# Performance work log

Measured on AMD Instinct MI355X. Metric: run time of the kernel, lower is better.

The kernel has to match this reference:

```python
import jax, jax.numpy as jnp
import numpy as np

MAX_DEPTH = 83.0
PI = 3.1415926535
SCALE = 8
FOCAL = 715.0

def setup_inputs() -> dict:
    key = jax.random.key(0)
    ks = jax.random.split(key, 16)
    B, C, H, W = 16, 128, 44, 152
    x = jax.random.normal(ks[0], (B, C, H, W), dtype=jnp.float32)
    # reduction 1x1 convs: 128->64->32->16->8->4
    chans = [128, 64, 32, 16, 8, 4]
    inp = {"x": x}
    for i in range(5):
        cin, cout = chans[i], chans[i + 1]
        w = jax.random.normal(ks[1 + 2 * i], (cout, cin), dtype=jnp.float32) * (1.0 / np.sqrt(cin))
        b = jax.random.normal(ks[2 + 2 * i], (cout,), dtype=jnp.float32) * 0.01
        inp[f"w{i}"] = w
        inp[f"b{i}"] = b
    # final 1x1 conv: 4 -> 3
    inp["cw"] = jax.random.normal(ks[11], (3, 4), dtype=jnp.float32) * 0.5
    inp["cb"] = jax.random.normal(ks[12], (3,), dtype=jnp.float32) * 0.01
    return inp

def _lpg_block(x, w0, b0, w1, b1, w2, b2, w3, b3, w4, b4, cw, cb):
    # reduction chain: 1x1 conv + ELU
    for w, b in ((w0, b0), (w1, b1), (w2, b2), (w3, b3), (w4, b4)):
        x = jax.nn.elu(jnp.einsum('oc,bchw->bohw', w, x) + b[None, :, None, None])
    # 4 -> 3 conv producing (theta, phi, dist) logits
    y = jnp.einsum('oc,bchw->bohw', cw, x) + cb[None, :, None, None]
    theta = jax.nn.sigmoid(y[:, 0]) * PI / 6.0          # [B,H,W]
    phi = jax.nn.sigmoid(y[:, 1]) * PI * 2.0
    dist = jax.nn.sigmoid(y[:, 2]) * MAX_DEPTH
    n1 = jnp.sin(theta) * jnp.cos(phi)
    n2 = jnp.sin(theta) * jnp.sin(phi)
    n3 = jnp.cos(theta)
    n = jnp.stack([n1, n2, n3], axis=1)                  # [B,3,H,W]
    # F.normalize(p=2, dim=1, eps=1e-12)
    norm = jnp.sqrt(jnp.sum(n * n, axis=1, keepdims=True))
    n = n / jnp.maximum(norm, 1e-12)
    n1, n2, n3 = n[:, 0], n[:, 1], n[:, 2]
    # LPG expansion: depth[b, y*s+ii, x*s+jj] = dist / (n1*u[jj] + n2*v[ii] + n3)
    s = SCALE
    off = (jnp.arange(s, dtype=jnp.float32) - (s - 1) / 2.0) / s / FOCAL  # [s]
    v = off[:, None]   # rows (ii)
    u = off[None, :]   # cols (jj)
    denom = (n1[..., None, None] * u + n2[..., None, None] * v
             + n3[..., None, None])                       # [B,H,W,s,s]
    depth = dist[..., None, None] / denom                 # [B,H,W,s,s]
    B, H, W = dist.shape
    depth = jnp.transpose(depth, (0, 1, 3, 2, 4)).reshape(B, 1, H * s, W * s)
    return depth

def reference(x, w0, b0, w1, b1, w2, b2, w3, b3, w4, b4, cw, cb):
    return _lpg_block(x, w0, b0, w1, b1, w2, b2, w3, b3, w4, b4, cw, cb)
```

## Files before the change

### kernel.cpp

```cpp
#include <hip/hip_runtime.h>
#include <math.h>

#define HW_   6688
#define W_    152
#define NPIX  107008
#define OW_   1216
#define OHW_  428032

typedef _Float16 f16;
typedef _Float16 f16x2 __attribute__((ext_vector_type(2)));
typedef _Float16 f16x4 __attribute__((ext_vector_type(4)));
typedef _Float16 f16x8 __attribute__((ext_vector_type(8)));
typedef float    f32x4 __attribute__((ext_vector_type(4)));

#define MFMA(a,b,c) __builtin_amdgcn_mfma_f32_16x16x32_f16((a),(b),(c),0,0,0)

#define SXH_STR  72
#define SA1_STR  40
#define SA2_OFF  5120
#define SA2_STR  24
#define SA3_OFF  8192
#define SA3_STR  16
#define SA0_OFF  10240
#define SA0_STR  72
#define LDSF16   19456

__device__ __forceinline__ float fast_sigmoid(float v) {
    return __builtin_amdgcn_rcpf(1.0f + __expf(-v));
}
__device__ __forceinline__ float eluf(float v) {
    return v > 0.0f ? v : (__expf(v) - 1.0f);
}
__device__ __forceinline__ void split8(const float* v, f16x8& hi, f16x8& lo) {
#pragma unroll
    for (int e = 0; e < 8; ++e) {
        f16 h = (f16)v[e];
        hi[e] = h;
        lo[e] = (f16)(v[e] - (float)h);
    }
}
__device__ __forceinline__ f16x4 elu_cvt4(f32x4 a) {
    f16x4 r;
    r[0] = (f16)eluf(a[0]); r[1] = (f16)eluf(a[1]);
    r[2] = (f16)eluf(a[2]); r[3] = (f16)eluf(a[3]);
    return r;
}
__device__ __forceinline__ void wave_fence() {
    __builtin_amdgcn_sched_barrier(0);
    __builtin_amdgcn_wave_barrier();
    __builtin_amdgcn_sched_barrier(0);
}
__device__ __forceinline__ void stage32(const float* __restrict__ xp, f16* dst) {
#pragma unroll 8
    for (int k = 0; k < 32; k += 2) {
        float v0 = xp[(size_t)k * HW_];
        float v1 = xp[(size_t)(k + 1) * HW_];
        f16x2 h; h[0] = (f16)v0; h[1] = (f16)v1;
        *(f16x2*)(dst + k) = h;
    }
}

__global__ __launch_bounds__(256, 4)
void lpg_mfma(const float* __restrict__ x,
              const float* __restrict__ w0, const float* __restrict__ b0,
              const float* __restrict__ w1, const float* __restrict__ b1,
              const float* __restrict__ w2, const float* __restrict__ b2,
              const float* __restrict__ w3, const float* __restrict__ b3,
              const float* __restrict__ w4, const float* __restrict__ b4,
              const float* __restrict__ cw, const float* __restrict__ cb,
              float* __restrict__ out) {
    __shared__ __align__(16) f16 S[LDSF16];
    f16* SX  = S;
    f16* SA0 = S + SA0_OFF;

    const int tid  = threadIdx.x;
    const int wv   = __builtin_amdgcn_readfirstlane(tid >> 6);
    const int lane = tid & 63;
    const int p    = lane & 15;
    const int q    = lane >> 4;
    const int pixbase = blockIdx.x * 128;

    const int i    = tid & 127;
    const int csub = (tid >> 7) * 32;
    int pixs = pixbase + i;
    int bbs  = pixs / HW_;
    int hws  = pixs - bbs * HW_;
    const float* xps = x + ((size_t)bbs * 128 + csub) * HW_ + hws;
    f16* dsts = SX + i * SXH_STR + csub;

    stage32(xps, dsts);

    const int w0row = (wv * 16 + p) * 128 + q * 8;
    f16x8 w0h[2], w0l[2];
#pragma unroll
    for (int kt = 0; kt < 2; ++kt) {
        float v[8];
#pragma unroll
        for (int e = 0; e < 8; ++e) v[e] = w0[w0row + kt * 32 + e];
        split8(v, w0h[kt], w0l[kt]);
    }
    f32x4 acc[8];
    {
        f32x4 b0v = *(const f32x4*)(b0 + wv * 16 + 4 * q);
#pragma unroll
        for (int t = 0; t < 8; ++t) acc[t] = b0v;
    }
    __syncthreads();

#pragma unroll 2
    for (int t = 0; t < 8; ++t) {
        const f16* bp = SX + (t * 16 + p) * SXH_STR + q * 8;
        f16x8 bf0 = *(const f16x8*)(bp);
        f16x8 bf1 = *(const f16x8*)(bp + 32);
        acc[t] = MFMA(w0h[0], bf0, acc[t]); acc[t] = MFMA(w0l[0], bf0, acc[t]);
        acc[t] = MFMA(w0h[1], bf1, acc[t]); acc[t] = MFMA(w0l[1], bf1, acc[t]);
    }
    __syncthreads();

    stage32(xps + (size_t)64 * HW_, dsts);
#pragma unroll
    for (int kt = 0; kt < 2; ++kt) {
        float v[8];
#pragma unroll
        for (int e = 0; e < 8; ++e) v[e] = w0[w0row + 64 + kt * 32 + e];
        split8(v, w0h[kt], w0l[kt]);
    }
    __syncthreads();

#pragma unroll 2
    for (int t = 0; t < 8; ++t) {
        const f16* bp = SX + (t * 16 + p) * SXH_STR + q * 8;
        f16x8 bf0 = *(const f16x8*)(bp);
        f16x8 bf1 = *(const f16x8*)(bp + 32);
        acc[t] = MFMA(w0h[0], bf0, acc[t]); acc[t] = MFMA(w0l[0], bf0, acc[t]);
        acc[t] = MFMA(w0h[1], bf1, acc[t]); acc[t] = MFMA(w0l[1], bf1, acc[t]);
        *(f16x4*)(SA0 + (t * 16 + p) * SA0_STR + wv * 16 + 4 * q) = elu_cvt4(acc[t]);
    }
    __syncthreads();

    f16x8 w1h[2][2], w1l[2][2];
#pragma unroll
    for (int Mt = 0; Mt < 2; ++Mt)
#pragma unroll
        for (int kt = 0; kt < 2; ++kt) {
            float v[8];
#pragma unroll
            for (int e = 0; e < 8; ++e) v[e] = w1[(Mt * 16 + p) * 64 + kt * 32 + q * 8 + e];
            split8(v, w1h[Mt][kt], w1l[Mt][kt]);
        }
    f16x8 w2h, w2l;
    {
        float v[8];
#pragma unroll
        for (int e = 0; e < 8; ++e) v[e] = w2[p * 32 + q * 8 + e];
        split8(v, w2h, w2l);
    }
    f16x8 w3h, w3l;
    {
        float v[8];
        bool ok = (p < 8) && (q < 2);
#pragma unroll
        for (int e = 0; e < 8; ++e) v[e] = ok ? w3[p * 16 + q * 8 + e] : 0.0f;
        split8(v, w3h, w3l);
    }
    f16x8 w4h, w4l;
    {
        float v[8];
        bool ok = (p < 4) && (q == 0);
#pragma unroll
        for (int e = 0; e < 8; ++e) v[e] = ok ? w4[p * 8 + e] : 0.0f;
        split8(v, w4h, w4l);
    }
    f16x8 whh, whl;
    {
        float v[8];
        bool ok = (p < 3) && (q == 0);
#pragma unroll
        for (int e = 0; e < 8; ++e) v[e] = (ok && e < 4) ? cw[p * 4 + e] : 0.0f;
        split8(v, whh, whl);
    }
    const f32x4 z4 = {0.f, 0.f, 0.f, 0.f};
    f32x4 b1v0 = *(const f32x4*)(b1 + 4 * q);
    f32x4 b1v1 = *(const f32x4*)(b1 + 16 + 4 * q);
    f32x4 b2v  = *(const f32x4*)(b2 + 4 * q);
    f32x4 b3v  = *(const f32x4*)(b3 + (q & 1) * 4);
    f32x4 b4v  = *(const f32x4*)(b4);
    float cb0v = cb[0], cb1v = cb[1], cb2v = cb[2];

    const int i0a = wv * 32 + p;
    const int i0b = wv * 32 + 16 + p;

    {
        f32x4 cA0 = b1v0, cA1 = b1v1, cB0 = b1v0, cB1 = b1v1;
#pragma unroll
        for (int kt = 0; kt < 2; ++kt) {
            f16x8 bfA = *(const f16x8*)(SA0 + i0a * SA0_STR + kt * 32 + q * 8);
            f16x8 bfB = *(const f16x8*)(SA0 + i0b * SA0_STR + kt * 32 + q * 8);
            cA0 = MFMA(w1h[0][kt], bfA, cA0); cA0 = MFMA(w1l[0][kt], bfA, cA0);
            cA1 = MFMA(w1h[1][kt], bfA, cA1); cA1 = MFMA(w1l[1][kt], bfA, cA1);
            cB0 = MFMA(w1h[0][kt], bfB, cB0); cB0 = MFMA(w1l[0][kt], bfB, cB0);
            cB1 = MFMA(w1h[1][kt], bfB, cB1); cB1 = MFMA(w1l[1][kt], bfB, cB1);
        }
        *(f16x4*)(SX + i0a * SA1_STR + 4 * q)      = elu_cvt4(cA0);
        *(f16x4*)(SX + i0a * SA1_STR + 16 + 4 * q) = elu_cvt4(cA1);
        *(f16x4*)(SX + i0b * SA1_STR + 4 * q)      = elu_cvt4(cB0);
        *(f16x4*)(SX + i0b * SA1_STR + 16 + 4 * q) = elu_cvt4(cB1);
    }
    wave_fence();

    {
        f16x8 bfA = *(const f16x8*)(SX + i0a * SA1_STR + q * 8);
        f16x8 bfB = *(const f16x8*)(SX + i0b * SA1_STR + q * 8);
        f32x4 cA = b2v, cB = b2v;
        cA = MFMA(w2h, bfA, cA); cA = MFMA(w2l, bfA, cA);
        cB = MFMA(w2h, bfB, cB); cB = MFMA(w2l, bfB, cB);
        *(f16x4*)(SX + SA2_OFF + i0a * SA2_STR + 4 * q) = elu_cvt4(cA);
        *(f16x4*)(SX + SA2_OFF + i0b * SA2_STR + 4 * q) = elu_cvt4(cB);
    }
    wave_fence();

    {
        f16x8 bfA = *(const f16x8*)(SX + SA2_OFF + i0a * SA2_STR + (q & 1) * 8);
        f16x8 bfB = *(const f16x8*)(SX + SA2_OFF + i0b * SA2_STR + (q & 1) * 8);
        if (q >= 2) { bfA = (f16x8){}; bfB = (f16x8){}; }
        f32x4 cA = (q < 2) ? b3v : z4, cB = (q < 2) ? b3v : z4;
        cA = MFMA(w3h, bfA, cA); cA = MFMA(w3l, bfA, cA);
        cB = MFMA(w3h, bfB, cB); cB = MFMA(w3l, bfB, cB);
        if (q < 2) {
            *(f16x4*)(SX + SA3_OFF + i0a * SA3_STR + 4 * q) = elu_cvt4(cA);
            *(f16x4*)(SX + SA3_OFF + i0b * SA3_STR + 4 * q) = elu_cvt4(cB);
        }
    }
    wave_fence();

    f32x4 cyA, cyB;
    {
        f16x8 bfA = *(const f16x8*)(SX + SA3_OFF + i0a * SA3_STR);
        f16x8 bfB = *(const f16x8*)(SX + SA3_OFF + i0b * SA3_STR);
        if (q != 0) { bfA = (f16x8){}; bfB = (f16x8){}; }
        f32x4 cA = (q == 0) ? b4v : z4, cB = (q == 0) ? b4v : z4;
        cA = MFMA(w4h, bfA, cA); cA = MFMA(w4l, bfA, cA);
        cB = MFMA(w4h, bfB, cB); cB = MFMA(w4l, bfB, cB);

        f16x8 hA = (f16x8){}, hB = (f16x8){};
        if (q == 0) {
#pragma unroll
            for (int e = 0; e < 4; ++e) {
                hA[e] = (f16)eluf(cA[e]);
                hB[e] = (f16)eluf(cB[e]);
            }
        }
        cyA = z4; cyB = z4;
        if (q == 0) {
            cyA[0] = cb0v; cyA[1] = cb1v; cyA[2] = cb2v;
            cyB[0] = cb0v; cyB[1] = cb1v; cyB[2] = cb2v;
        }
        cyA = MFMA(whh, hA, cyA); cyA = MFMA(whl, hA, cyA);
        cyB = MFMA(whh, hB, cyB); cyB = MFMA(whl, hB, cyB);
    }

#pragma unroll
    for (int nt = 0; nt < 2; ++nt) {
        const int i0 = wv * 32 + nt * 16 + p;
        float y0 = __shfl(nt ? cyB[0] : cyA[0], p);
        float y1 = __shfl(nt ? cyB[1] : cyA[1], p);
        float y2 = __shfl(nt ? cyB[2] : cyA[2], p);

        float theta = 0.5235987756f * fast_sigmoid(y0);
        float phi   = 6.2831853072f * fast_sigmoid(y1);
        float dist  = 83.0f         * fast_sigmoid(y2);
        float st = __sinf(theta), ct = __cosf(theta);
        float sp = __sinf(phi),   cp = __cosf(phi);
        float n1 = st * cp, n2 = st * sp, n3 = ct;
        float inv = __frsqrt_rn(fmaf(n1, n1, fmaf(n2, n2, n3 * n3)));
        n1 *= inv; n2 *= inv; n3 *= inv;

        const float ksc = 1.0f / (8.0f * 715.0f);
        float nu[8];
#pragma unroll
        for (int j = 0; j < 8; ++j) nu[j] = n1 * (((float)j - 3.5f) * ksc);

        int pix = pixbase + i0;
        int bb  = pix / HW_;
        int hw  = pix - bb * HW_;
        int hh  = hw / W_;
        int ww  = hw - hh * W_;
        const int obase = bb * OHW_ + (hh * 8) * OW_ + ww * 8;
#pragma unroll
        for (int r = 0; r < 2; ++r) {
            int irow = q * 2 + r;
            float base = fmaf(n2, ((float)irow - 3.5f) * ksc, n3);
            float4 r0, r1;
            r0.x = dist * __builtin_amdgcn_rcpf(base + nu[0]);
            r0.y = dist * __builtin_amdgcn_rcpf(base + nu[1]);
            r0.z = dist * __builtin_amdgcn_rcpf(base + nu[2]);
            r0.w = dist * __builtin_amdgcn_rcpf(base + nu[3]);
            r1.x = dist * __builtin_amdgcn_rcpf(base + nu[4]);
            r1.y = dist * __builtin_amdgcn_rcpf(base + nu[5]);
            r1.z = dist * __builtin_amdgcn_rcpf(base + nu[6]);
            r1.w = dist * __builtin_amdgcn_rcpf(base + nu[7]);
            float4* op = (float4*)(out + obase + irow * OW_);
            op[0] = r0;
            op[1] = r1;
        }
    }
}

extern "C" void kernel_launch(void* const* d_in, const int* in_sizes, int n_in,
                              void* d_out, int out_size, void* d_ws, size_t ws_size,
                              hipStream_t stream) {
    const float* x  = (const float*)d_in[0];
    const float* w0 = (const float*)d_in[1];
    const float* b0 = (const float*)d_in[2];
    const float* w1 = (const float*)d_in[3];
    const float* b1 = (const float*)d_in[4];
    const float* w2 = (const float*)d_in[5];
    const float* b2 = (const float*)d_in[6];
    const float* w3 = (const float*)d_in[7];
    const float* b3 = (const float*)d_in[8];
    const float* w4 = (const float*)d_in[9];
    const float* b4 = (const float*)d_in[10];
    const float* cw = (const float*)d_in[11];
    const float* cb = (const float*)d_in[12];
    float* outp = (float*)d_out;

    lpg_mfma<<<NPIX / 128, 256, 0, stream>>>(x, w0, b0, w1, b1, w2, b2, w3, b3,
                                             w4, b4, cw, cb, outp);
}
```

Baseline: 30.91 us.

## Pre-split weights in a prep kernel and prefetch both input halves

Adds a small prep kernel that splits all conv weights into fp16 hi/lo pairs, including zero padding, and writes them to workspace. The main kernel then loads them as vectors instead of redoing scalar loads and splits in every block. The main kernel also issues all 64 channel loads per thread up front so the second half overlaps the first MFMA pass, and converts with packed RTZ conversions. It drops the explicit zero masking, relying on the padded weights instead. The costs are an extra kernel launch and much higher register pressure from holding 64 floats per thread, which may hurt occupancy or cause spills.

```diff
diff --git a/kernel.cpp b/kernel.cpp
--- a/kernel.cpp
+++ b/kernel.cpp
@@ -14,6 +14,14 @@
 typedef float    f32x4 __attribute__((ext_vector_type(4)));
 
 #define MFMA(a,b,c) __builtin_amdgcn_mfma_f32_16x16x32_f16((a),(b),(c),0,0,0)
+
+#define WS_W0 0
+#define WS_W1 8192
+#define WS_W2 10240
+#define WS_W3 10752
+#define WS_W4 11264
+#define WS_CW 11776
+#define WS_LO 12288
 
 #define SXH_STR  72
 #define SA1_STR  40
@@ -31,14 +39,6 @@
 __device__ __forceinline__ float eluf(float v) {
     return v > 0.0f ? v : (__expf(v) - 1.0f);
 }
-__device__ __forceinline__ void split8(const float* v, f16x8& hi, f16x8& lo) {
-#pragma unroll
-    for (int e = 0; e < 8; ++e) {
-        f16 h = (f16)v[e];
-        hi[e] = h;
-        lo[e] = (f16)(v[e] - (float)h);
-    }
-}
 __device__ __forceinline__ f16x4 elu_cvt4(f32x4 a) {
     f16x4 r;
     r[0] = (f16)eluf(a[0]); r[1] = (f16)eluf(a[1]);
@@ -50,28 +50,70 @@
     __builtin_amdgcn_wave_barrier();
     __builtin_amdgcn_sched_barrier(0);
 }
-__device__ __forceinline__ void stage32(const float* __restrict__ xp, f16* dst) {
-#pragma unroll 8
-    for (int k = 0; k < 32; k += 2) {
-        float v0 = xp[(size_t)k * HW_];
-        float v1 = xp[(size_t)(k + 1) * HW_];
-        f16x2 h; h[0] = (f16)v0; h[1] = (f16)v1;
-        *(f16x2*)(dst + k) = h;
+
+__global__ void prep_split(const float* __restrict__ w0, const float* __restrict__ w1,
+                           const float* __restrict__ w2, const float* __restrict__ w3,
+                           const float* __restrict__ w4, const float* __restrict__ cw,
+                           f16* __restrict__ hi) {
+    f16* lo = hi + WS_LO;
+    int t = blockIdx.x * 256 + threadIdx.x;
+    int stride = gridDim.x * 256;
+    for (int i = t; i < 8192; i += stride) {
+        float v = w0[i]; f16 h = (f16)v;
+        hi[WS_W0 + i] = h; lo[WS_W0 + i] = (f16)(v - (float)h);
+    }
+    for (int i = t; i < 2048; i += stride) {
+        float v = w1[i]; f16 h = (f16)v;
+        hi[WS_W1 + i] = h; lo[WS_W1 + i] = (f16)(v - (float)h);
+    }
+    for (int i = t; i < 512; i += stride) {
+        float v = w2[i]; f16 h = (f16)v;
+        hi[WS_W2 + i] = h; lo[WS_W2 + i] = (f16)(v - (float)h);
+    }
+    for (int i = t; i < 512; i += stride) {
+        int p = i >> 5, c = i & 31, q = c >> 3, e = c & 7;
+        float v = (p < 8 && q < 2) ? w3[p * 16 + q * 8 + e] : 0.0f;
+        f16 h = (f16)v;
+        hi[WS_W3 + i] = h; lo[WS_W3 + i] = (f16)(v - (float)h);
+    }
+    for (int i = t; i < 512; i += stride) {
+        int p = i >> 5, c = i & 31, q = c >> 3, e = c & 7;
+        float v = (p < 4 && q == 0) ? w4[p * 8 + e] : 0.0f;
+        f16 h = (f16)v;
+        hi[WS_W4 + i] = h; lo[WS_W4 + i] = (f16)(v - (float)h);
+    }
+    for (int i = t; i < 512; i += stride) {
+        int p = i >> 5, c = i & 31, q = c >> 3, e = c & 7;
+        float v = (p < 3 && q == 0 && e < 4) ? cw[p * 4 + e] : 0.0f;
+        f16 h = (f16)v;
+        hi[WS_CW + i] = h; lo[WS_CW + i] = (f16)(v - (float)h);
+    }
+}
+
+__device__ __forceinline__ void pack_write32(const float* v, f16* dst) {
+#pragma unroll
+    for (int g = 0; g < 4; ++g) {
+        f16x8 h;
+#pragma unroll
+        for (int e = 0; e < 8; e += 2) {
+            auto pk = __builtin_amdgcn_cvt_pkrtz(v[g * 8 + e], v[g * 8 + e + 1]);
+            h[e] = pk[0]; h[e + 1] = pk[1];
+        }
+        *(f16x8*)(dst + g * 8) = h;
     }
 }
 
 __global__ __launch_bounds__(256, 4)
-void lpg_mfma(const float* __restrict__ x,
-              const float* __restrict__ w0, const float* __restrict__ b0,
-              const float* __restrict__ w1, const float* __restrict__ b1,
-              const float* __restrict__ w2, const float* __restrict__ b2,
-              const float* __restrict__ w3, const float* __restrict__ b3,
-              const float* __restrict__ w4, const float* __restrict__ b4,
-              const float* __restrict__ cw, const float* __restrict__ cb,
+void lpg_mfma(const float* __restrict__ x, const f16* __restrict__ wsp,
+              const float* __restrict__ b0, const float* __restrict__ b1,
+              const float* __restrict__ b2, const float* __restrict__ b3,
+              const float* __restrict__ b4, const float* __restrict__ cb,
               float* __restrict__ out) {
     __shared__ __align__(16) f16 S[LDSF16];
     f16* SX  = S;
     f16* SA0 = S + SA0_OFF;
+    const f16* whi = wsp;
+    const f16* wlo = wsp + WS_LO;
 
     const int tid  = threadIdx.x;
     const int wv   = __builtin_amdgcn_readfirstlane(tid >> 6);
@@ -88,16 +130,20 @@
     const float* xps = x + ((size_t)bbs * 128 + csub) * HW_ + hws;
     f16* dsts = SX + i * SXH_STR + csub;
 
-    stage32(xps, dsts);
+    float v0[32], v1[32];
+#pragma unroll
+    for (int k = 0; k < 32; ++k) v0[k] = xps[(size_t)k * HW_];
+#pragma unroll
+    for (int k = 0; k < 32; ++k) v1[k] = xps[(size_t)(k + 64) * HW_];
+
+    pack_write32(v0, dsts);
 
     const int w0row = (wv * 16 + p) * 128 + q * 8;
     f16x8 w0h[2], w0l[2];
 #pragma unroll
     for (int kt = 0; kt < 2; ++kt) {
-        float v[8];
-#pragma unroll
-        for (int e = 0; e < 8; ++e) v[e] = w0[w0row + kt * 32 + e];
-        split8(v, w0h[kt], w0l[kt]);
+        w0h[kt] = *(const f16x8*)(whi + WS_W0 + w0row + kt * 32);
+        w0l[kt] = *(const f16x8*)(wlo + WS_W0 + w0row + kt * 32);
     }
     f32x4 acc[8];
     {
@@ -117,13 +163,11 @@
     }
     __syncthreads();
 
-    stage32(xps + (size_t)64 * HW_, dsts);
+    pack_write32(v1, dsts);
 #pragma unroll
     for (int kt = 0; kt < 2; ++kt) {
-        float v[8];
-#pragma unroll
-        for (int e = 0; e < 8; ++e) v[e] = w0[w0row + 64 + kt * 32 + e];
-        split8(v, w0h[kt], w0l[kt]);
+        w0h[kt] = *(const f16x8*)(whi + WS_W0 + w0row + 64 + kt * 32);
+        w0l[kt] = *(const f16x8*)(wlo + WS_W0 + w0row + 64 + kt * 32);
     }
     __syncthreads();
 
@@ -143,42 +187,20 @@
     for (int Mt = 0; Mt < 2; ++Mt)
 #pragma unroll
         for (int kt = 0; kt < 2; ++kt) {
-            float v[8];
-#pragma unroll
-            for (int e = 0; e < 8; ++e) v[e] = w1[(Mt * 16 + p) * 64 + kt * 32 + q * 8 + e];
-            split8(v, w1h[Mt][kt], w1l[Mt][kt]);
-        }
-    f16x8 w2h, w2l;
-    {
-        float v[8];
-#pragma unroll
-        for (int e = 0; e < 8; ++e) v[e] = w2[p * 32 + q * 8 + e];
-        split8(v, w2h, w2l);
-    }
-    f16x8 w3h, w3l;
-    {
-        float v[8];
-        bool ok = (p < 8) && (q < 2);
-#pragma unroll
-        for (int e = 0; e < 8; ++e) v[e] = ok ? w3[p * 16 + q * 8 + e] : 0.0f;
-        split8(v, w3h, w3l);
-    }
-    f16x8 w4h, w4l;
-    {
-        float v[8];
-        bool ok = (p < 4) && (q == 0);
-#pragma unroll
-        for (int e = 0; e < 8; ++e) v[e] = ok ? w4[p * 8 + e] : 0.0f;
-        split8(v, w4h, w4l);
-    }
-    f16x8 whh, whl;
-    {
-        float v[8];
-        bool ok = (p < 3) && (q == 0);
-#pragma unroll
-        for (int e = 0; e < 8; ++e) v[e] = (ok && e < 4) ? cw[p * 4 + e] : 0.0f;
-        split8(v, whh, whl);
-    }
+            int idx = WS_W1 + (Mt * 16 + p) * 64 + kt * 32 + q * 8;
+            w1h[Mt][kt] = *(const f16x8*)(whi + idx);
+            w1l[Mt][kt] = *(const f16x8*)(wlo + idx);
+        }
+    const int fidx = p * 32 + q * 8;
+    f16x8 w2h = *(const f16x8*)(whi + WS_W2 + fidx);
+    f16x8 w2l = *(const f16x8*)(wlo + WS_W2 + fidx);
+    f16x8 w3h = *(const f16x8*)(whi + WS_W3 + fidx);
+    f16x8 w3l = *(const f16x8*)(wlo + WS_W3 + fidx);
+    f16x8 w4h = *(const f16x8*)(whi + WS_W4 + fidx);
+    f16x8 w4l = *(const f16x8*)(wlo + WS_W4 + fidx);
+    f16x8 whh = *(const f16x8*)(whi + WS_CW + fidx);
+    f16x8 whl = *(const f16x8*)(wlo + WS_CW + fidx);
+
     const f32x4 z4 = {0.f, 0.f, 0.f, 0.f};
     f32x4 b1v0 = *(const f32x4*)(b1 + 4 * q);
     f32x4 b1v1 = *(const f32x4*)(b1 + 16 + 4 * q);
@@ -222,8 +244,7 @@
     {
         f16x8 bfA = *(const f16x8*)(SX + SA2_OFF + i0a * SA2_STR + (q & 1) * 8);
         f16x8 bfB = *(const f16x8*)(SX + SA2_OFF + i0b * SA2_STR + (q & 1) * 8);
-        if (q >= 2) { bfA = (f16x8){}; bfB = (f16x8){}; }
-        f32x4 cA = (q < 2) ? b3v : z4, cB = (q < 2) ? b3v : z4;
+        f32x4 cA = b3v, cB = b3v;
         cA = MFMA(w3h, bfA, cA); cA = MFMA(w3l, bfA, cA);
         cB = MFMA(w3h, bfB, cB); cB = MFMA(w3l, bfB, cB);
         if (q < 2) {
@@ -237,8 +258,7 @@
     {
         f16x8 bfA = *(const f16x8*)(SX + SA3_OFF + i0a * SA3_STR);
         f16x8 bfB = *(const f16x8*)(SX + SA3_OFF + i0b * SA3_STR);
-        if (q != 0) { bfA = (f16x8){}; bfB = (f16x8){}; }
-        f32x4 cA = (q == 0) ? b4v : z4, cB = (q == 0) ? b4v : z4;
+        f32x4 cA = b4v, cB = b4v;
         cA = MFMA(w4h, bfA, cA); cA = MFMA(w4l, bfA, cA);
         cB = MFMA(w4h, bfB, cB); cB = MFMA(w4l, bfB, cB);
 
@@ -322,8 +342,9 @@
     const float* b4 = (const float*)d_in[10];
     const float* cw = (const float*)d_in[11];
     const float* cb = (const float*)d_in[12];
+    f16* wsp   = (f16*)d_ws;
     float* outp = (float*)d_out;
 
-    lpg_mfma<<<NPIX / 128, 256, 0, stream>>>(x, w0, b0, w1, b1, w2, b2, w3, b3,
-                                             w4, b4, cw, cb, outp);
-}
+    prep_split<<<32, 256, 0, stream>>>(w0, w1, w2, w3, w4, cw, wsp);
+    lpg_mfma<<<NPIX / 128, 256, 0, stream>>>(x, wsp, b0, b1, b2, b3, b4, cb, outp);
+}
```

New measurement: 32.35 us. +4.7%, slower.

## Load layer-0 activations directly into registers per wave, removing LDS staging and barriers

Applied to the files above, without the earlier changes.

Layer 0 is restructured so that each wave computes all 64 output channels for its own 32 pixels. The B operand is loaded straight from global memory into registers and converted with packed conversion, with a double-buffered prefetch of the next K chunk. This removes the LDS staging of x and the block-wide __syncthreads barriers, and replaces the last one with a wave-level fence. The trade-off is that each wave now reloads and re-splits all of the w0 weights per K chunk, which raises register pressure and redundant weight loads. The per-lane global loads are strided by HW, so coalescing is only 16 pixels wide per instruction.

```diff
diff --git a/kernel.cpp b/kernel.cpp
--- a/kernel.cpp
+++ b/kernel.cpp
@@ -15,14 +15,14 @@
 
 #define MFMA(a,b,c) __builtin_amdgcn_mfma_f32_16x16x32_f16((a),(b),(c),0,0,0)
 
-#define SXH_STR  72
+#define SA0_OFF  0
+#define SA0_STR  72
+#define SA1_OFF  9216
 #define SA1_STR  40
-#define SA2_OFF  5120
+#define SA2_OFF  14336
 #define SA2_STR  24
-#define SA3_OFF  8192
+#define SA3_OFF  17408
 #define SA3_STR  16
-#define SA0_OFF  10240
-#define SA0_STR  72
 #define LDSF16   19456
 
 __device__ __forceinline__ float fast_sigmoid(float v) {
@@ -38,6 +38,15 @@
         hi[e] = h;
         lo[e] = (f16)(v[e] - (float)h);
     }
+}
+__device__ __forceinline__ f16x8 cvt8(const float* v) {
+    f16x8 r;
+#pragma unroll
+    for (int e = 0; e < 8; e += 2) {
+        auto pk = __builtin_amdgcn_cvt_pkrtz(v[e], v[e + 1]);
+        r[e] = (f16)pk[0]; r[e + 1] = (f16)pk[1];
+    }
+    return r;
 }
 __device__ __forceinline__ f16x4 elu_cvt4(f32x4 a) {
     f16x4 r;
@@ -49,15 +58,6 @@
     __builtin_amdgcn_sched_barrier(0);
     __builtin_amdgcn_wave_barrier();
     __builtin_amdgcn_sched_barrier(0);
-}
-__device__ __forceinline__ void stage32(const float* __restrict__ xp, f16* dst) {
-#pragma unroll 8
-    for (int k = 0; k < 32; k += 2) {
-        float v0 = xp[(size_t)k * HW_];
-        float v1 = xp[(size_t)(k + 1) * HW_];
-        f16x2 h; h[0] = (f16)v0; h[1] = (f16)v1;
-        *(f16x2*)(dst + k) = h;
-    }
 }
 
 __global__ __launch_bounds__(256, 4)
@@ -70,8 +70,6 @@
               const float* __restrict__ cw, const float* __restrict__ cb,
               float* __restrict__ out) {
     __shared__ __align__(16) f16 S[LDSF16];
-    f16* SX  = S;
-    f16* SA0 = S + SA0_OFF;
 
     const int tid  = threadIdx.x;
     const int wv   = __builtin_amdgcn_readfirstlane(tid >> 6);
@@ -80,63 +78,60 @@
     const int q    = lane >> 4;
     const int pixbase = blockIdx.x * 128;
 
-    const int i    = tid & 127;
-    const int csub = (tid >> 7) * 32;
-    int pixs = pixbase + i;
-    int bbs  = pixs / HW_;
-    int hws  = pixs - bbs * HW_;
-    const float* xps = x + ((size_t)bbs * 128 + csub) * HW_ + hws;
-    f16* dsts = SX + i * SXH_STR + csub;
-
-    stage32(xps, dsts);
-
-    const int w0row = (wv * 16 + p) * 128 + q * 8;
-    f16x8 w0h[2], w0l[2];
-#pragma unroll
-    for (int kt = 0; kt < 2; ++kt) {
-        float v[8];
-#pragma unroll
-        for (int e = 0; e < 8; ++e) v[e] = w0[w0row + kt * 32 + e];
-        split8(v, w0h[kt], w0l[kt]);
-    }
-    f32x4 acc[8];
-    {
-        f32x4 b0v = *(const f32x4*)(b0 + wv * 16 + 4 * q);
-#pragma unroll
-        for (int t = 0; t < 8; ++t) acc[t] = b0v;
-    }
-    __syncthreads();
-
-#pragma unroll 2
-    for (int t = 0; t < 8; ++t) {
-        const f16* bp = SX + (t * 16 + p) * SXH_STR + q * 8;
-        f16x8 bf0 = *(const f16x8*)(bp);
-        f16x8 bf1 = *(const f16x8*)(bp + 32);
-        acc[t] = MFMA(w0h[0], bf0, acc[t]); acc[t] = MFMA(w0l[0], bf0, acc[t]);
-        acc[t] = MFMA(w0h[1], bf1, acc[t]); acc[t] = MFMA(w0l[1], bf1, acc[t]);
-    }
-    __syncthreads();
-
-    stage32(xps + (size_t)64 * HW_, dsts);
-#pragma unroll
-    for (int kt = 0; kt < 2; ++kt) {
-        float v[8];
-#pragma unroll
-        for (int e = 0; e < 8; ++e) v[e] = w0[w0row + 64 + kt * 32 + e];
-        split8(v, w0h[kt], w0l[kt]);
-    }
-    __syncthreads();
-
-#pragma unroll 2
-    for (int t = 0; t < 8; ++t) {
-        const f16* bp = SX + (t * 16 + p) * SXH_STR + q * 8;
-        f16x8 bf0 = *(const f16x8*)(bp);
-        f16x8 bf1 = *(const f16x8*)(bp + 32);
-        acc[t] = MFMA(w0h[0], bf0, acc[t]); acc[t] = MFMA(w0l[0], bf0, acc[t]);
-        acc[t] = MFMA(w0h[1], bf1, acc[t]); acc[t] = MFMA(w0l[1], bf1, acc[t]);
-        *(f16x4*)(SA0 + (t * 16 + p) * SA0_STR + wv * 16 + 4 * q) = elu_cvt4(acc[t]);
-    }
-    __syncthreads();
+    const int i0a = wv * 32 + p;
+    const int i0b = wv * 32 + 16 + p;
+
+    const int pixA = pixbase + i0a;
+    const int pixB = pixbase + i0b;
+    const int bbA = pixA / HW_, hwA = pixA - bbA * HW_;
+    const int bbB = pixB / HW_, hwB = pixB - bbB * HW_;
+    const float* xA = x + ((size_t)bbA * 128 + q * 8) * HW_ + hwA;
+    const float* xB = x + ((size_t)bbB * 128 + q * 8) * HW_ + hwB;
+
+    f32x4 acc[4][2];
+#pragma unroll
+    for (int Mt = 0; Mt < 4; ++Mt) {
+        f32x4 b0v = *(const f32x4*)(b0 + Mt * 16 + 4 * q);
+        acc[Mt][0] = b0v; acc[Mt][1] = b0v;
+    }
+
+    float vA[2][8], vB[2][8];
+#pragma unroll
+    for (int e = 0; e < 8; ++e) {
+        vA[0][e] = xA[(size_t)e * HW_];
+        vB[0][e] = xB[(size_t)e * HW_];
+    }
+#pragma unroll
+    for (int kt = 0; kt < 4; ++kt) {
+        const int cur = kt & 1, nxt = cur ^ 1;
+        if (kt < 3) {
+#pragma unroll
+            for (int e = 0; e < 8; ++e) {
+                vA[nxt][e] = xA[(size_t)((kt + 1) * 32 + e) * HW_];
+                vB[nxt][e] = xB[(size_t)((kt + 1) * 32 + e) * HW_];
+            }
+        }
+        f16x8 bfA = cvt8(vA[cur]);
+        f16x8 bfB = cvt8(vB[cur]);
+#pragma unroll
+        for (int Mt = 0; Mt < 4; ++Mt) {
+            const float* wr = w0 + (Mt * 16 + p) * 128 + kt * 32 + q * 8;
+            float w8[8];
+#pragma unroll
+            for (int e = 0; e < 8; ++e) w8[e] = wr[e];
+            f16x8 wh, wl; split8(w8, wh, wl);
+            acc[Mt][0] = MFMA(wh, bfA, acc[Mt][0]);
+            acc[Mt][0] = MFMA(wl, bfA, acc[Mt][0]);
+            acc[Mt][1] = MFMA(wh, bfB, acc[Mt][1]);
+            acc[Mt][1] = MFMA(wl, bfB, acc[Mt][1]);
+        }
+    }
+#pragma unroll
+    for (int Mt = 0; Mt < 4; ++Mt) {
+        *(f16x4*)(S + SA0_OFF + i0a * SA0_STR + Mt * 16 + 4 * q) = elu_cvt4(acc[Mt][0]);
+        *(f16x4*)(S + SA0_OFF + i0b * SA0_STR + Mt * 16 + 4 * q) = elu_cvt4(acc[Mt][1]);
+    }
+    wave_fence();
 
     f16x8 w1h[2][2], w1l[2][2];
 #pragma unroll
@@ -187,56 +182,53 @@
     f32x4 b4v  = *(const f32x4*)(b4);
     float cb0v = cb[0], cb1v = cb[1], cb2v = cb[2];
 
-    const int i0a = wv * 32 + p;
-    const int i0b = wv * 32 + 16 + p;
-
     {
         f32x4 cA0 = b1v0, cA1 = b1v1, cB0 = b1v0, cB1 = b1v1;
 #pragma unroll
         for (int kt = 0; kt < 2; ++kt) {
-            f16x8 bfA = *(const f16x8*)(SA0 + i0a * SA0_STR + kt * 32 + q * 8);
-            f16x8 bfB = *(const f16x8*)(SA0 + i0b * SA0_STR + kt * 32 + q * 8);
+            f16x8 bfA = *(const f16x8*)(S + SA0_OFF + i0a * SA0_STR + kt * 32 + q * 8);
+            f16x8 bfB = *(const f16x8*)(S + SA0_OFF + i0b * SA0_STR + kt * 32 + q * 8);
             cA0 = MFMA(w1h[0][kt], bfA, cA0); cA0 = MFMA(w1l[0][kt], bfA, cA0);
             cA1 = MFMA(w1h[1][kt], bfA, cA1); cA1 = MFMA(w1l[1][kt], bfA, cA1);
             cB0 = MFMA(w1h[0][kt], bfB, cB0); cB0 = MFMA(w1l[0][kt], bfB, cB0);
             cB1 = MFMA(w1h[1][kt], bfB, cB1); cB1 = MFMA(w1l[1][kt], bfB, cB1);
         }
-        *(f16x4*)(SX + i0a * SA1_STR + 4 * q)      = elu_cvt4(cA0);
-        *(f16x4*)(SX + i0a * SA1_STR + 16 + 4 * q) = elu_cvt4(cA1);
-        *(f16x4*)(SX + i0b * SA1_STR + 4 * q)      = elu_cvt4(cB0);
-        *(f16x4*)(SX + i0b * SA1_STR + 16 + 4 * q) = elu_cvt4(cB1);
+        *(f16x4*)(S + SA1_OFF + i0a * SA1_STR + 4 * q)      = elu_cvt4(cA0);
+        *(f16x4*)(S + SA1_OFF + i0a * SA1_STR + 16 + 4 * q) = elu_cvt4(cA1);
+        *(f16x4*)(S + SA1_OFF + i0b * SA1_STR + 4 * q)      = elu_cvt4(cB0);
+        *(f16x4*)(S + SA1_OFF + i0b * SA1_STR + 16 + 4 * q) = elu_cvt4(cB1);
     }
     wave_fence();
 
     {
-        f16x8 bfA = *(const f16x8*)(SX + i0a * SA1_STR + q * 8);
-        f16x8 bfB = *(const f16x8*)(SX + i0b * SA1_STR + q * 8);
+        f16x8 bfA = *(const f16x8*)(S + SA1_OFF + i0a * SA1_STR + q * 8);
+        f16x8 bfB = *(const f16x8*)(S + SA1_OFF + i0b * SA1_STR + q * 8);
         f32x4 cA = b2v, cB = b2v;
         cA = MFMA(w2h, bfA, cA); cA = MFMA(w2l, bfA, cA);
         cB = MFMA(w2h, bfB, cB); cB = MFMA(w2l, bfB, cB);
-        *(f16x4*)(SX + SA2_OFF + i0a * SA2_STR + 4 * q) = elu_cvt4(cA);
-        *(f16x4*)(SX + SA2_OFF + i0b * SA2_STR + 4 * q) = elu_cvt4(cB);
+        *(f16x4*)(S + SA2_OFF + i0a * SA2_STR + 4 * q) = elu_cvt4(cA);
+        *(f16x4*)(S + SA2_OFF + i0b * SA2_STR + 4 * q) = elu_cvt4(cB);
     }
     wave_fence();
 
     {
-        f16x8 bfA = *(const f16x8*)(SX + SA2_OFF + i0a * SA2_STR + (q & 1) * 8);
-        f16x8 bfB = *(const f16x8*)(SX + SA2_OFF + i0b * SA2_STR + (q & 1) * 8);
+        f16x8 bfA = *(const f16x8*)(S + SA2_OFF + i0a * SA2_STR + (q & 1) * 8);
+        f16x8 bfB = *(const f16x8*)(S + SA2_OFF + i0b * SA2_STR + (q & 1) * 8);
         if (q >= 2) { bfA = (f16x8){}; bfB = (f16x8){}; }
         f32x4 cA = (q < 2) ? b3v : z4, cB = (q < 2) ? b3v : z4;
         cA = MFMA(w3h, bfA, cA); cA = MFMA(w3l, bfA, cA);
         cB = MFMA(w3h, bfB, cB); cB = MFMA(w3l, bfB, cB);
         if (q < 2) {
-            *(f16x4*)(SX + SA3_OFF + i0a * SA3_STR + 4 * q) = elu_cvt4(cA);
-            *(f16x4*)(SX + SA3_OFF + i0b * SA3_STR + 4 * q) = elu_cvt4(cB);
+            *(f16x4*)(S + SA3_OFF + i0a * SA3_STR + 4 * q) = elu_cvt4(cA);
+            *(f16x4*)(S + SA3_OFF + i0b * SA3_STR + 4 * q) = elu_cvt4(cB);
         }
     }
     wave_fence();
 
     f32x4 cyA, cyB;
     {
-        f16x8 bfA = *(const f16x8*)(SX + SA3_OFF + i0a * SA3_STR);
-        f16x8 bfB = *(const f16x8*)(SX + SA3_OFF + i0b * SA3_STR);
+        f16x8 bfA = *(const f16x8*)(S + SA3_OFF + i0a * SA3_STR);
+        f16x8 bfB = *(const f16x8*)(S + SA3_OFF + i0b * SA3_STR);
         if (q != 0) { bfA = (f16x8){}; bfB = (f16x8){}; }
         f32x4 cA = (q == 0) ? b4v : z4, cB = (q == 0) ? b4v : z4;
         cA = MFMA(w4h, bfA, cA); cA = MFMA(w4l, bfA, cA);
```

Measured after the change: 36.09 us. +16.8%, slower.
